# Performance work log

Hardware: AMD Instinct MI355X
Metric: run time of the kernel (lower is better)

## Reference

```python
import jax, jax.numpy as jnp
import numpy as np

R = 32
BN_EPS = 1e-5


def _bn(x, g, b):
    # eval-mode BatchNorm with running_mean=0, running_var=1
    shp = (1, -1) + (1,) * (x.ndim - 2)
    scale = g / np.float32(np.sqrt(1.0 + BN_EPS))
    return x * scale.reshape(shp) + b.reshape(shp)


def _conv3d(x, w, b):
    y = jax.lax.conv_general_dilated(x, w, (1, 1, 1), [(1, 1)] * 3,
                                     dimension_numbers=('NCDHW', 'OIDHW', 'NCDHW'))
    return y + b[None, :, None, None, None]


def _conv1d(x, w, b):  # kernel_size=1 conv -> matmul; w [O,I], x [B,I,N]
    return jnp.einsum('oi,bin->bon', w, x) + b[None, :, None]


def _voxelize(features, coords, r):
    # PVCNN Voxelization: detach coords, center, normalize, scatter-average
    coords = jax.lax.stop_gradient(coords)
    c = coords - coords.mean(axis=2, keepdims=True)            # [B,3,N]
    nrm = jnp.linalg.norm(c, axis=1, keepdims=True)            # [B,1,N]
    c = c / (nrm.max(axis=2, keepdims=True) * 2.0) + 0.5
    c = jnp.clip(c * r, 0.0, r - 1.0)                          # float voxel coords
    vox = jnp.round(c).astype(jnp.int32)
    B, C, N = features.shape
    idx = vox[:, 0] * r * r + vox[:, 1] * r + vox[:, 2]        # [B,N]
    flat = (idx + (jnp.arange(B, dtype=jnp.int32) * (r ** 3))[:, None]).reshape(-1)
    feats = features.transpose(0, 2, 1).reshape(B * N, C)
    sums = jax.ops.segment_sum(feats, flat, num_segments=B * r ** 3)
    cnt = jax.ops.segment_sum(jnp.ones((B * N,), features.dtype), flat, num_segments=B * r ** 3)
    grid = sums / jnp.maximum(cnt, 1.0)[:, None]
    grid = grid.reshape(B, r, r, r, C).transpose(0, 4, 1, 2, 3)  # [B,C,r,r,r]
    return grid, c


def _devoxelize(grid, c, r):
    # trilinear interpolation gather at float coords c in [0, r-1]
    B, C = grid.shape[:2]
    lo = jnp.clip(jnp.floor(c).astype(jnp.int32), 0, r - 1)
    hi = jnp.minimum(lo + 1, r - 1)
    f = c - lo.astype(c.dtype)
    gridf = grid.reshape(B, C, r * r * r)
    gather = jax.vmap(lambda g, i: g[:, i])  # per-batch [C,R3],[N] -> [C,N]
    out = jnp.zeros((B, C, c.shape[2]), grid.dtype)
    for ix, wx in ((lo[:, 0], 1.0 - f[:, 0]), (hi[:, 0], f[:, 0])):
        for iy, wy in ((lo[:, 1], 1.0 - f[:, 1]), (hi[:, 1], f[:, 1])):
            for iz, wz in ((lo[:, 2], 1.0 - f[:, 2]), (hi[:, 2], f[:, 2])):
                idx = ix * r * r + iy * r + iz
                out = out + gather(gridf, idx) * (wx * wy * wz)[:, None, :]
    return out


def setup_inputs() -> dict:
    key = jax.random.key(0)
    ks = jax.random.split(key, 24)
    n = lambda k, s, sc=0.05: (jax.random.normal(k, s, dtype=jnp.float32) * sc)
    inp = {
        'features': jax.random.normal(ks[0], (4, 64, 65536), dtype=jnp.float32),
        'coords': jax.random.normal(ks[1], (4, 3, 65536), dtype=jnp.float32),
        'vconv_w': n(ks[2], (64, 64, 3, 3, 3)),
        'vconv_b': n(ks[3], (64,)),
        'vbn_g': 1.0 + n(ks[4], (64,)),
        'vbn_b': n(ks[5], (64,)),
        'res_w': n(ks[6], (2, 2, 64, 64, 3, 3, 3)),
        'res_b': n(ks[7], (2, 2, 64)),
        'res_bn_g': 1.0 + n(ks[8], (2, 2, 64)),
        'res_bn_b': n(ks[9], (2, 2, 64)),
        'pf_w': n(ks[10], (64, 64)),
        'pf_b': n(ks[11], (64,)),
        'pf_bn_g': 1.0 + n(ks[12], (64,)),
        'pf_bn_b': n(ks[13], (64,)),
        'attn_wa': n(ks[14], (16, 64)),
        'attn_ba': n(ks[15], (16,)),
        'attn_wb': n(ks[16], (16, 64)),
        'attn_bb': n(ks[17], (16,)),
        'attn_wc': n(ks[18], (1, 32)),
        'attn_bc': n(ks[19], (1,)),
    }
    return inp


def reference(features, coords, vconv_w, vconv_b, vbn_g, vbn_b,
              res_w, res_b, res_bn_g, res_bn_b,
              pf_w, pf_b, pf_bn_g, pf_bn_b,
              attn_wa, attn_ba, attn_wb, attn_bb, attn_wc, attn_bc):
    grid, nc = _voxelize(features, coords, R)
    # BasicConvolutionBlock
    x = jax.nn.relu(_bn(_conv3d(grid, vconv_w, vconv_b), vbn_g, vbn_b))
    # two ResidualBlocks (inc==outc, stride 1 -> identity downsample)
    for i in range(2):
        y = jax.nn.relu(_bn(_conv3d(x, res_w[i, 0], res_b[i, 0]), res_bn_g[i, 0], res_bn_b[i, 0]))
        y = _bn(_conv3d(y, res_w[i, 1], res_b[i, 1]), res_bn_g[i, 1], res_bn_b[i, 1])
        x = jax.nn.relu(y + x)
    vfeat = _devoxelize(x, nc, R)                               # [B,64,N]
    # SharedMLP: Conv1d(k=1) + BN1d + ReLU
    pfeat = jax.nn.relu(_bn(_conv1d(features, pf_w, pf_b), pf_bn_g, pf_bn_b))
    # Attn fusion (channel dim 64 -> atten_64 branch)
    xa = _conv1d(vfeat, attn_wa, attn_ba)
    xb = _conv1d(pfeat, attn_wb, attn_bb)
    q = _conv1d(jnp.concatenate([xa, xb], axis=1), attn_wc, attn_bc)
    attention = 1.0 + jax.nn.sigmoid(q)
    fused = vfeat * attention + pfeat
    return fused
```

## Files before the change

kernel.cpp:

```cpp
#include <hip/hip_runtime.h>
#include <math.h>

#define NPT 65536
#define NB 4
#define R3 32768

typedef __attribute__((ext_vector_type(8))) short short8;
typedef __attribute__((ext_vector_type(16))) float f32x16;

#define OFF_WB16 0
#define OFF_BEFF 276480
#define OFF_PWB  276800
#define OFF_PB   280896
#define OFF_WAE  280960
#define OFF_WBE  281024
#define OFF_Q0   281088
#define OFF_MEAN 281104
#define OFF_MAXN 281116
#define OFF_PART 281120
#define OFF_AUX  281248
#define OFF_CB3  281504
#define OFF_CUR  1067936
#define OFF_ORD  1199008
#define OFF_GA   1330080
#define OFF_G0   9718688
#define OFF_G1   13912992

__device__ __forceinline__ unsigned short f2b(float f) {
    union { float f; unsigned int u; } v; v.f = f;
    unsigned int r = v.u + 0x7fffu + ((v.u >> 16) & 1u);
    return (unsigned short)(r >> 16);
}
__device__ __forceinline__ float b2f(unsigned short u) {
    union { unsigned int u; float f; } v; v.u = ((unsigned int)u) << 16; return v.f;
}

__global__ void k_fold_w(const float* __restrict__ vconv_w, const float* __restrict__ vbn_g,
                         const float* __restrict__ res_w, const float* __restrict__ res_bn_g,
                         unsigned short* __restrict__ wb16) {
    int idx = blockIdx.x * 256 + threadIdx.x;
    if (idx >= 5 * 27 * 4 * 2 * 64 * 8) return;
    int j = idx & 7;
    int l = (idx >> 3) & 63;
    int nh = (idx >> 9) & 1;
    int ks = (idx >> 10) & 3;
    int rest = idx >> 12;
    int t = rest % 27;
    int layer = rest / 27;
    int i = ks * 16 + ((l >> 5) << 3) + j;
    int o = nh * 32 + (l & 31);
    const float invs = rsqrtf(1.00001f);
    float scale, wsrc;
    if (layer == 0) {
        scale = vbn_g[o] * invs;
        wsrc = vconv_w[(o * 64 + i) * 27 + t];
    } else {
        scale = res_bn_g[(layer - 1) * 64 + o] * invs;
        wsrc = res_w[(size_t)(layer - 1) * 110592 + (o * 64 + i) * 27 + t];
    }
    wb16[idx] = f2b(wsrc * scale);
}

__global__ void k_misc(const float* __restrict__ vconv_b, const float* __restrict__ vbn_g,
                       const float* __restrict__ vbn_b,
                       const float* __restrict__ res_b, const float* __restrict__ res_bn_g,
                       const float* __restrict__ res_bn_b,
                       const float* __restrict__ pf_w, const float* __restrict__ pf_b,
                       const float* __restrict__ pf_bn_g, const float* __restrict__ pf_bn_b,
                       const float* __restrict__ wa, const float* __restrict__ ba,
                       const float* __restrict__ wb, const float* __restrict__ bb,
                       const float* __restrict__ wc, const float* __restrict__ bc,
                       float* __restrict__ ws) {
    int idx = blockIdx.x * 256 + threadIdx.x;
    const float invs = rsqrtf(1.00001f);
    if (idx < 320) {
        int l = idx >> 6, o = idx & 63;
        float b_, g_, s_;
        if (l == 0) { b_ = vconv_b[o]; g_ = vbn_g[o]; s_ = vbn_b[o]; }
        else {
            b_ = res_b[(l - 1) * 64 + o];
            g_ = res_bn_g[(l - 1) * 64 + o];
            s_ = res_bn_b[(l - 1) * 64 + o];
        }
        ws[OFF_BEFF + idx] = b_ * g_ * invs + s_;
    } else if (idx < 4416) {
        int e = idx - 320;
        int j = e & 7;
        int lane = (e >> 3) & 63;
        int ks = (e >> 9) & 3;
        int half = e >> 11;
        int i = ks * 16 + ((lane >> 5) << 3) + j;
        int o = half * 32 + (lane & 31);
        ((unsigned short*)(ws + OFF_PWB))[e] = f2b(pf_w[o * 64 + i] * pf_bn_g[o] * invs);
    } else if (idx < 4480) {
        int o = idx - 4416;
        ws[OFF_PB + o] = pf_b[o] * pf_bn_g[o] * invs + pf_bn_b[o];
    } else if (idx < 4544) {
        int o = idx - 4480;
        float s = 0.f;
        for (int j = 0; j < 16; j++) s += wc[j] * wa[j * 64 + o];
        ws[OFF_WAE + o] = s;
    } else if (idx < 4608) {
        int o = idx - 4544;
        float s = 0.f;
        for (int j = 0; j < 16; j++) s += wc[16 + j] * wb[j * 64 + o];
        ws[OFF_WBE + o] = s;
    } else if (idx == 4608) {
        float s = bc[0];
        for (int j = 0; j < 16; j++) s += wc[j] * ba[j] + wc[16 + j] * bb[j];
        ws[OFF_Q0] = s;
    }
}

__global__ void k_zero(float4* __restrict__ p, int n4) {
    int i = blockIdx.x * 256 + threadIdx.x;
    if (i < n4) p[i] = make_float4(0.f, 0.f, 0.f, 0.f);
}

__global__ __launch_bounds__(256) void k_mean1(const float* __restrict__ coords,
                                               float* __restrict__ part) {
    __shared__ float sm[256];
    int bd = blockIdx.x >> 3, chunk = blockIdx.x & 7;
    int tid = threadIdx.x;
    const float* p = coords + (size_t)bd * NPT + chunk * 8192;
    float s = 0.f;
    for (int n = tid; n < 8192; n += 256) s += p[n];
    sm[tid] = s; __syncthreads();
    for (int st = 128; st > 0; st >>= 1) {
        if (tid < st) sm[tid] += sm[tid + st];
        __syncthreads();
    }
    if (tid == 0) part[blockIdx.x] = sm[0];
}

__global__ void k_mean2(const float* __restrict__ part, float* __restrict__ mean) {
    int t = threadIdx.x;
    if (t < 12) {
        float s = 0.f;
        for (int c = 0; c < 8; c++) s += part[t * 8 + c];
        mean[t] = s * (1.0f / NPT);
    }
}

__global__ __launch_bounds__(256) void k_maxn1(const float* __restrict__ coords,
                                               const float* __restrict__ mean,
                                               float* __restrict__ part) {
    __shared__ float sm[256];
    int b = blockIdx.x >> 3, chunk = blockIdx.x & 7;
    int tid = threadIdx.x;
    float m0 = mean[b * 3], m1 = mean[b * 3 + 1], m2 = mean[b * 3 + 2];
    const float* p0 = coords + (size_t)(b * 3) * NPT + chunk * 8192;
    float mx = 0.f;
    for (int n = tid; n < 8192; n += 256) {
        float dx = p0[n] - m0, dy = p0[NPT + n] - m1, dz = p0[2 * NPT + n] - m2;
        mx = fmaxf(mx, dx * dx + dy * dy + dz * dz);
    }
    sm[tid] = mx; __syncthreads();
    for (int st = 128; st > 0; st >>= 1) {
        if (tid < st) sm[tid] = fmaxf(sm[tid], sm[tid + st]);
        __syncthreads();
    }
    if (tid == 0) part[96 + blockIdx.x] = sm[0];
}

__global__ void k_maxn2(const float* __restrict__ part, float* __restrict__ maxn) {
    int t = threadIdx.x;
    if (t < 4) {
        float m = 0.f;
        for (int c = 0; c < 8; c++) m = fmaxf(m, part[96 + t * 8 + c]);
        maxn[t] = sqrtf(m);
    }
}

__global__ void k_prep(const float* __restrict__ coords, const float* __restrict__ mean,
                       const float* __restrict__ maxn, float* __restrict__ cb3,
                       int* __restrict__ cursor) {
    int gid = blockIdx.x * 256 + threadIdx.x;
    int b = gid >> 16, n = gid & 65535;
    float inv = 0.5f / maxn[b];
    float c0 = (coords[(size_t)(b * 3) * NPT + n]     - mean[b * 3])     * inv + 0.5f;
    float c1 = (coords[(size_t)(b * 3 + 1) * NPT + n] - mean[b * 3 + 1]) * inv + 0.5f;
    float c2 = (coords[(size_t)(b * 3 + 2) * NPT + n] - mean[b * 3 + 2]) * inv + 0.5f;
    c0 = fminf(fmaxf(c0 * 32.f, 0.f), 31.f);
    c1 = fminf(fmaxf(c1 * 32.f, 0.f), 31.f);
    c2 = fminf(fmaxf(c2 * 32.f, 0.f), 31.f);
    cb3[gid * 3]     = c0;
    cb3[gid * 3 + 1] = c1;
    cb3[gid * 3 + 2] = c2;
    int vx = b * R3 + ((int)rintf(c0) * 1024 + (int)rintf(c1) * 32 + (int)rintf(c2));
    atomicAdd(&cursor[vx], 1);
}

__global__ void k_scan1(int* __restrict__ cur, int* __restrict__ aux) {
    __shared__ int sm[256];
    int t = threadIdx.x;
    int base = blockIdx.x * 512 + t * 2;
    int c0 = cur[base], c1 = cur[base + 1];
    int s = c0 + c1;
    sm[t] = s; __syncthreads();
    for (int off = 1; off < 256; off <<= 1) {
        int v = (t >= off) ? sm[t - off] : 0;
        __syncthreads();
        sm[t] += v;
        __syncthreads();
    }
    int ex = sm[t] - s;
    cur[base] = ex;
    cur[base + 1] = ex + c0;
    if (t == 255) aux[blockIdx.x] = sm[t];
}

__global__ void k_scan2(int* __restrict__ aux) {
    __shared__ int sm[256];
    int t = threadIdx.x;
    int v0 = aux[t];
    sm[t] = v0; __syncthreads();
    for (int off = 1; off < 256; off <<= 1) {
        int v = (t >= off) ? sm[t - off] : 0;
        __syncthreads();
        sm[t] += v;
        __syncthreads();
    }
    aux[t] = sm[t] - v0;
}

__global__ void k_scan3(int* __restrict__ cur, const int* __restrict__ aux) {
    int t = threadIdx.x;
    int add = aux[blockIdx.x];
    int base = blockIdx.x * 512 + t * 2;
    cur[base] += add;
    cur[base + 1] += add;
}

__global__ __launch_bounds__(256) void k_trans(const float* __restrict__ feats,
                                               unsigned short* __restrict__ ft) {
    __shared__ float lds[64][65];
    int b = blockIdx.x >> 10;
    int n0 = (blockIdx.x & 1023) << 6;
    int tid = threadIdx.x;
    int nl = tid & 63;
    #pragma unroll
    for (int it = 0; it < 16; it++) {
        int ch = it * 4 + (tid >> 6);
        lds[nl][ch] = feats[((size_t)(b * 64 + ch) << 16) + n0 + nl];
    }
    __syncthreads();
    int nn = tid >> 2;
    int ch0 = (tid & 3) << 4;
    size_t obase = (((size_t)(b << 16) + n0 + nn) << 6) + ch0;
    short8 v0, v1;
    #pragma unroll
    for (int j = 0; j < 8; j++) v0[j] = (short)f2b(lds[nn][ch0 + j]);
    #pragma unroll
    for (int j = 0; j < 8; j++) v1[j] = (short)f2b(lds[nn][ch0 + 8 + j]);
    *(short8*)(ft + obase) = v0;
    *(short8*)(ft + obase + 8) = v1;
}

__global__ void k_place(const float* __restrict__ cb3, int* __restrict__ cursor,
                        unsigned short* __restrict__ order) {
    int gid = blockIdx.x * 256 + threadIdx.x;
    int b = gid >> 16;
    float c0 = cb3[gid * 3], c1 = cb3[gid * 3 + 1], c2 = cb3[gid * 3 + 2];
    int vx = b * R3 + ((int)rintf(c0) * 1024 + (int)rintf(c1) * 32 + (int)rintf(c2));
    int slot = atomicAdd(&cursor[vx], 1);
    order[slot] = (unsigned short)(gid & 65535);
}

__global__ __launch_bounds__(256) void k_gather(const int* __restrict__ cursor,
        const unsigned short* __restrict__ order, const unsigned short* __restrict__ ft,
        unsigned short* __restrict__ g0) {
    int tid = threadIdx.x;
    int lane = tid & 63;
    int vx = blockIdx.x * 4 + (tid >> 6);
    int e = cursor[vx];
    int s = (vx == 0) ? 0 : cursor[vx - 1];
    int cnt = e - s;
    int p = lane >> 3;
    int g = lane & 7;
    int bb = vx >> 15;
    float acc[8] = {0.f, 0.f, 0.f, 0.f, 0.f, 0.f, 0.f, 0.f};
    for (int base = s; base < e; base += 8) {
        int idx = base + p;
        if (idx < e) {
            int n = order[idx];
            const unsigned short* fp = ft + (((size_t)(bb << 16) + n) << 6) + (g << 3);
            short8 v = *(const short8*)fp;
            #pragma unroll
            for (int j = 0; j < 8; j++) acc[j] += b2f((unsigned short)v[j]);
        }
    }
    #pragma unroll
    for (int j = 0; j < 8; j++) {
        acc[j] += __shfl_xor(acc[j], 8, 64);
        acc[j] += __shfl_xor(acc[j], 16, 64);
        acc[j] += __shfl_xor(acc[j], 32, 64);
    }
    if (p == 0) {
        float inv = 1.0f / (float)max(cnt, 1);
        int col = vx >> 5, z = vx & 31;
        short8 o8;
        #pragma unroll
        for (int j = 0; j < 8; j++) o8[j] = (short)f2b(acc[j] * inv);
        *(short8*)(g0 + (size_t)col * 2048 + (g << 8) + z * 8) = o8;
    }
}

__global__ __launch_bounds__(256) void k_conv(const unsigned short* __restrict__ in,
        const unsigned short* __restrict__ w, const float* __restrict__ bias,
        const float* __restrict__ idF, float* __restrict__ outF,
        unsigned short* __restrict__ out) {
    __shared__ unsigned short sA[18 * 2048];
    int tid = threadIdx.x;
    int lane = tid & 63;
    int wid = tid >> 6;
    int cp = wid & 1;
    int nh = wid >> 1;
    int tile = blockIdx.x;
    int b = blockIdx.y;
    int x = tile >> 3;
    int y0 = (tile & 7) << 2;
    #pragma unroll 1
    for (int s = 0; s < 18; s++) {
        int gx = x + s / 6 - 1;
        int gy = y0 + s % 6 - 1;
        if ((unsigned)gx < 32u && (unsigned)gy < 32u) {
            const unsigned short* gsrc = in + (((size_t)b * 1024 + gx * 32 + gy) << 11)
                                            + ((size_t)tid << 3);
            __builtin_amdgcn_global_load_lds(
                (const __attribute__((address_space(1))) unsigned int*)gsrc,
                (__attribute__((address_space(3))) unsigned int*)(sA + s * 2048 + (wid << 9)),
                16, 0, 0);
        } else {
            ((float4*)(sA + s * 2048))[tid] = make_float4(0.f, 0.f, 0.f, 0.f);
        }
    }
    __syncthreads();
    f32x16 accA = {}, accB = {};
    const short8 zero8 = {0, 0, 0, 0, 0, 0, 0, 0};
    int half = lane >> 5;
    #pragma unroll 1
    for (int t = 0; t < 27; t++) {
        int dxi = t / 9, dyi = (t / 3) % 3, dz = t % 3 - 1;
        int s0 = dxi * 6 + dyi + cp * 2;
        int zz = (lane & 31) + dz;
        bool zv = (unsigned)zz < 32u;
        int zc = zv ? zz : 0;
        const unsigned short* ac = sA + s0 * 2048 + (half << 8) + zc * 8;
        const unsigned short* wp = w + t * 4096 + nh * 512 + lane * 8;
        #pragma unroll
        for (int ks = 0; ks < 4; ks++) {
            short8 bf = *(const short8*)(wp + ks * 1024);
            short8 a0 = *(const short8*)(ac + ks * 512);
            short8 a1 = *(const short8*)(ac + 2048 + ks * 512);
            if (!zv) { a0 = zero8; a1 = zero8; }
            accA = __builtin_amdgcn_mfma_f32_32x32x16_bf16(a0, bf, accA, 0, 0, 0);
            accB = __builtin_amdgcn_mfma_f32_32x32x16_bf16(a1, bf, accB, 0, 0, 0);
        }
    }
    int o = nh * 32 + (lane & 31);
    float bb = bias[o];
    #pragma unroll
    for (int cc = 0; cc < 2; cc++) {
        int outcol = b * 1024 + x * 32 + (y0 + cp * 2 + cc);
        size_t obase = ((size_t)outcol << 11) + (size_t)((o >> 3) << 8) + (o & 7);
        const f32x16& acc = cc ? accB : accA;
        #pragma unroll
        for (int r = 0; r < 16; r++) {
            int z = (r & 3) + ((r >> 2) << 3) + ((lane >> 5) << 2);
            size_t oe = obase + (size_t)z * 8;
            float v = acc[r] + bb;
            if (idF) v += idF[oe];
            v = fmaxf(v, 0.f);
            out[oe] = f2b(v);
            if (outF) outF[oe] = v;
        }
    }
}

__global__ __launch_bounds__(256) void k_pfeat(const float* __restrict__ feats,
        const float* __restrict__ pb, const unsigned short* __restrict__ pwb,
        unsigned short* __restrict__ pf) {
    int tid = threadIdx.x;
    int lane = tid & 63;
    int wv = tid >> 6;
    int tile = blockIdx.x * 4 + wv;
    int b = tile >> 11;
    int n0 = (tile & 2047) << 5;
    int m = lane & 31, kg = lane >> 5;
    const float* fb = feats + ((size_t)b << 22) + n0 + m;
    f32x16 acc0 = {}, acc1 = {};
    #pragma unroll
    for (int ks = 0; ks < 4; ks++) {
        short8 af;
        #pragma unroll
        for (int j = 0; j < 8; j++)
            af[j] = (short)f2b(fb[(size_t)(ks * 16 + kg * 8 + j) << 16]);
        short8 b0 = *(const short8*)(pwb + ((size_t)(ks * 64 + lane) << 3));
        short8 b1 = *(const short8*)(pwb + ((size_t)((4 + ks) * 64 + lane) << 3));
        acc0 = __builtin_amdgcn_mfma_f32_32x32x16_bf16(af, b0, acc0, 0, 0, 0);
        acc1 = __builtin_amdgcn_mfma_f32_32x32x16_bf16(af, b1, acc1, 0, 0, 0);
    }
    int och = lane & 31;
    float bias0 = pb[och], bias1 = pb[32 + och];
    #pragma unroll
    for (int r = 0; r < 16; r++) {
        int p = (r & 3) + ((r >> 2) << 3) + ((lane >> 5) << 2);
        size_t base = ((size_t)(b << 16) + n0 + p) << 6;
        pf[base + och]      = f2b(fmaxf(acc0[r] + bias0, 0.f));
        pf[base + 32 + och] = f2b(fmaxf(acc1[r] + bias1, 0.f));
    }
}

__global__ __launch_bounds__(256) void k_final(const float* __restrict__ cb3,
        const unsigned short* __restrict__ gb, const unsigned short* __restrict__ pfeat,
        const float* __restrict__ ws, float* __restrict__ out) {
    __shared__ float sq[256];
    int tid = threadIdx.x;
    int p = tid & 31;
    int g = tid >> 5;
    int b = blockIdx.y;
    int n = (blockIdx.x << 5) + p;
    int gid = (b << 16) + n;
    float c0 = cb3[gid * 3], c1 = cb3[gid * 3 + 1], c2 = cb3[gid * 3 + 2];
    int lx = (int)floorf(c0), ly = (int)floorf(c1), lz = (int)floorf(c2);
    int hx = min(lx + 1, 31), hy = min(ly + 1, 31), hz = min(lz + 1, 31);
    float fx = c0 - (float)lx, fy = c1 - (float)ly, fz = c2 - (float)lz;
    int xs[2] = {lx, hx}; float wxx[2] = {1.f - fx, fx};
    int ys[2] = {ly, hy}; float wyy[2] = {1.f - fy, fy};
    int zs[2] = {lz, hz}; float wzz[2] = {1.f - fz, fz};
    float vf[8];
    #pragma unroll
    for (int j = 0; j < 8; j++) vf[j] = 0.f;
    #pragma unroll
    for (int ii = 0; ii < 2; ii++)
    #pragma unroll
    for (int jj = 0; jj < 2; jj++)
    #pragma unroll
    for (int kk = 0; kk < 2; kk++) {
        float wgt = wxx[ii] * wyy[jj] * wzz[kk];
        const unsigned short* gp = gb + (((size_t)b * 1024 + xs[ii] * 32 + ys[jj]) << 11)
                                      + (g << 8) + zs[kk] * 8;
        short8 v = *(const short8*)gp;
        #pragma unroll
        for (int j = 0; j < 8; j++) vf[j] += wgt * b2f((unsigned short)v[j]);
    }
    float pfv[8];
    const unsigned short* pp = pfeat + ((size_t)gid << 6) + (g << 3);
    short8 pv = *(const short8*)pp;
    #pragma unroll
    for (int j = 0; j < 8; j++) pfv[j] = b2f((unsigned short)pv[j]);
    const float* wae = ws + OFF_WAE + (g << 3);
    const float* wbe = ws + OFF_WBE + (g << 3);
    float part = 0.f;
    #pragma unroll
    for (int j = 0; j < 8; j++) part += wae[j] * vf[j] + wbe[j] * pfv[j];
    sq[tid] = part;
    __syncthreads();
    float q = ws[OFF_Q0];
    #pragma unroll
    for (int gg = 0; gg < 8; gg++) q += sq[(gg << 5) + p];
    float attn = 1.0f + 1.0f / (1.0f + expf(-q));
    float* op = out + (((size_t)(b * 64 + (g << 3))) << 16) + n;
    #pragma unroll
    for (int j = 0; j < 8; j++) op[(size_t)j << 16] = vf[j] * attn + pfv[j];
}

extern "C" void kernel_launch(void* const* d_in, const int* in_sizes, int n_in,
                              void* d_out, int out_size, void* d_ws, size_t ws_size,
                              hipStream_t stream) {
    const float* features = (const float*)d_in[0];
    const float* coords   = (const float*)d_in[1];
    const float* vconv_w  = (const float*)d_in[2];
    const float* vconv_b  = (const float*)d_in[3];
    const float* vbn_g    = (const float*)d_in[4];
    const float* vbn_b    = (const float*)d_in[5];
    const float* res_w    = (const float*)d_in[6];
    const float* res_b    = (const float*)d_in[7];
    const float* res_bn_g = (const float*)d_in[8];
    const float* res_bn_b = (const float*)d_in[9];
    const float* pf_w     = (const float*)d_in[10];
    const float* pf_b     = (const float*)d_in[11];
    const float* pf_bn_g  = (const float*)d_in[12];
    const float* pf_bn_b  = (const float*)d_in[13];
    const float* attn_wa  = (const float*)d_in[14];
    const float* attn_ba  = (const float*)d_in[15];
    const float* attn_wb  = (const float*)d_in[16];
    const float* attn_bb  = (const float*)d_in[17];
    const float* attn_wc  = (const float*)d_in[18];
    const float* attn_bc  = (const float*)d_in[19];
    float* ws  = (float*)d_ws;
    float* out = (float*)d_out;

    unsigned short* WB  = (unsigned short*)(ws + OFF_WB16);
    unsigned short* PWB = (unsigned short*)(ws + OFF_PWB);
    int*            CUR = (int*)(ws + OFF_CUR);
    int*            AUX = (int*)(ws + OFF_AUX);
    unsigned short* ORD = (unsigned short*)(ws + OFF_ORD);
    unsigned short* FT  = (unsigned short*)(ws + OFF_GA);
    unsigned short* PF  = (unsigned short*)(ws + OFF_GA);
    float* GA = ws + OFF_GA;
    unsigned short* G0 = (unsigned short*)(ws + OFF_G0);
    unsigned short* G1 = (unsigned short*)(ws + OFF_G1);
    const float* Bv = ws + OFF_BEFF;

    k_fold_w<<<2160, 256, 0, stream>>>(vconv_w, vbn_g, res_w, res_bn_g, WB);
    k_misc<<<19, 256, 0, stream>>>(vconv_b, vbn_g, vbn_b, res_b, res_bn_g, res_bn_b,
                                   pf_w, pf_b, pf_bn_g, pf_bn_b,
                                   attn_wa, attn_ba, attn_wb, attn_bb, attn_wc, attn_bc, ws);
    k_zero<<<128, 256, 0, stream>>>((float4*)CUR, 32768);
    k_mean1<<<96, 256, 0, stream>>>(coords, ws + OFF_PART);
    k_mean2<<<1, 64, 0, stream>>>(ws + OFF_PART, ws + OFF_MEAN);
    k_maxn1<<<32, 256, 0, stream>>>(coords, ws + OFF_MEAN, ws + OFF_PART);
    k_maxn2<<<1, 64, 0, stream>>>(ws + OFF_PART, ws + OFF_MAXN);
    k_prep<<<1024, 256, 0, stream>>>(coords, ws + OFF_MEAN, ws + OFF_MAXN,
                                     ws + OFF_CB3, CUR);
    k_scan1<<<256, 256, 0, stream>>>(CUR, AUX);
    k_scan2<<<1, 256, 0, stream>>>(AUX);
    k_scan3<<<256, 256, 0, stream>>>(CUR, AUX);
    k_trans<<<4096, 256, 0, stream>>>(features, FT);
    k_place<<<1024, 256, 0, stream>>>(ws + OFF_CB3, CUR, ORD);
    k_gather<<<32768, 256, 0, stream>>>(CUR, ORD, FT, G0);

    dim3 cg(256, 4);
    k_conv<<<cg, 256, 0, stream>>>(G0, WB + 0 * 110592, Bv + 0,   nullptr, GA,      G1);
    k_conv<<<cg, 256, 0, stream>>>(G1, WB + 1 * 110592, Bv + 64,  nullptr, nullptr, G0);
    k_conv<<<cg, 256, 0, stream>>>(G0, WB + 2 * 110592, Bv + 128, GA,      GA,      G1);
    k_conv<<<cg, 256, 0, stream>>>(G1, WB + 3 * 110592, Bv + 192, nullptr, nullptr, G0);
    k_conv<<<cg, 256, 0, stream>>>(G0, WB + 4 * 110592, Bv + 256, GA,      nullptr, G1);

    k_pfeat<<<2048, 256, 0, stream>>>(features, ws + OFF_PB, PWB, PF);

    dim3 fg(2048, 4);
    k_final<<<fg, 256, 0, stream>>>(ws + OFF_CB3, G1, PF, ws, out);
}
```

Baseline: 563.5 us.

## Write final conv output z-major and reduce attention logits with wave shuffles

```diff
diff --git a/kernel.cpp b/kernel.cpp
--- a/kernel.cpp
+++ b/kernel.cpp
@@ -309,7 +309,7 @@
 __global__ __launch_bounds__(256) void k_conv(const unsigned short* __restrict__ in,
         const unsigned short* __restrict__ w, const float* __restrict__ bias,
         const float* __restrict__ idF, float* __restrict__ outF,
-        unsigned short* __restrict__ out) {
+        unsigned short* __restrict__ out, int zmaj) {
     __shared__ unsigned short sA[18 * 2048];
     int tid = threadIdx.x;
     int lane = tid & 63;
@@ -363,7 +363,8 @@
     #pragma unroll
     for (int cc = 0; cc < 2; cc++) {
         int outcol = b * 1024 + x * 32 + (y0 + cp * 2 + cc);
-        size_t obase = ((size_t)outcol << 11) + (size_t)((o >> 3) << 8) + (o & 7);
+        size_t cbase = (size_t)outcol << 11;
+        size_t obase = cbase + (size_t)((o >> 3) << 8) + (o & 7);
         const f32x16& acc = cc ? accB : accA;
         #pragma unroll
         for (int r = 0; r < 16; r++) {
@@ -372,7 +373,8 @@
             float v = acc[r] + bb;
             if (idF) v += idF[oe];
             v = fmaxf(v, 0.f);
-            out[oe] = f2b(v);
+            if (zmaj) out[cbase + (size_t)z * 64 + o] = f2b(v);
+            else out[oe] = f2b(v);
             if (outF) outF[oe] = v;
         }
     }
@@ -415,12 +417,12 @@
 __global__ __launch_bounds__(256) void k_final(const float* __restrict__ cb3,
         const unsigned short* __restrict__ gb, const unsigned short* __restrict__ pfeat,
         const float* __restrict__ ws, float* __restrict__ out) {
-    __shared__ float sq[256];
-    int tid = threadIdx.x;
-    int p = tid & 31;
-    int g = tid >> 5;
+    int tid = threadIdx.x;
+    int lane = tid & 63;
+    int g = lane >> 3;
+    int p = lane & 7;
     int b = blockIdx.y;
-    int n = (blockIdx.x << 5) + p;
+    int n = (blockIdx.x << 5) + ((tid >> 6) << 3) + p;
     int gid = (b << 16) + n;
     float c0 = cb3[gid * 3], c1 = cb3[gid * 3 + 1], c2 = cb3[gid * 3 + 2];
     int lx = (int)floorf(c0), ly = (int)floorf(c1), lz = (int)floorf(c2);
@@ -440,7 +442,7 @@
     for (int kk = 0; kk < 2; kk++) {
         float wgt = wxx[ii] * wyy[jj] * wzz[kk];
         const unsigned short* gp = gb + (((size_t)b * 1024 + xs[ii] * 32 + ys[jj]) << 11)
-                                      + (g << 8) + zs[kk] * 8;
+                                      + zs[kk] * 64 + (g << 3);
         short8 v = *(const short8*)gp;
         #pragma unroll
         for (int j = 0; j < 8; j++) vf[j] += wgt * b2f((unsigned short)v[j]);
@@ -455,11 +457,10 @@
     float part = 0.f;
     #pragma unroll
     for (int j = 0; j < 8; j++) part += wae[j] * vf[j] + wbe[j] * pfv[j];
-    sq[tid] = part;
-    __syncthreads();
-    float q = ws[OFF_Q0];
-    #pragma unroll
-    for (int gg = 0; gg < 8; gg++) q += sq[(gg << 5) + p];
+    part += __shfl_xor(part, 8, 64);
+    part += __shfl_xor(part, 16, 64);
+    part += __shfl_xor(part, 32, 64);
+    float q = part + ws[OFF_Q0];
     float attn = 1.0f + 1.0f / (1.0f + expf(-q));
     float* op = out + (((size_t)(b * 64 + (g << 3))) << 16) + n;
     #pragma unroll
@@ -523,11 +524,11 @@
     k_gather<<<32768, 256, 0, stream>>>(CUR, ORD, FT, G0);
 
     dim3 cg(256, 4);
-    k_conv<<<cg, 256, 0, stream>>>(G0, WB + 0 * 110592, Bv + 0,   nullptr, GA,      G1);
-    k_conv<<<cg, 256, 0, stream>>>(G1, WB + 1 * 110592, Bv + 64,  nullptr, nullptr, G0);
-    k_conv<<<cg, 256, 0, stream>>>(G0, WB + 2 * 110592, Bv + 128, GA,      GA,      G1);
-    k_conv<<<cg, 256, 0, stream>>>(G1, WB + 3 * 110592, Bv + 192, nullptr, nullptr, G0);
-    k_conv<<<cg, 256, 0, stream>>>(G0, WB + 4 * 110592, Bv + 256, GA,      nullptr, G1);
+    k_conv<<<cg, 256, 0, stream>>>(G0, WB + 0 * 110592, Bv + 0,   nullptr, GA,      G1, 0);
+    k_conv<<<cg, 256, 0, stream>>>(G1, WB + 1 * 110592, Bv + 64,  nullptr, nullptr, G0, 0);
+    k_conv<<<cg, 256, 0, stream>>>(G0, WB + 2 * 110592, Bv + 128, GA,      GA,      G1, 0);
+    k_conv<<<cg, 256, 0, stream>>>(G1, WB + 3 * 110592, Bv + 192, nullptr, nullptr, G0, 0);
+    k_conv<<<cg, 256, 0, stream>>>(G0, WB + 4 * 110592, Bv + 256, GA,      nullptr, G1, 1);
 
     k_pfeat<<<2048, 256, 0, stream>>>(features, ws + OFF_PB, PWB, PF);
 
```

After: 554.5 us. About the same (-1.6%).
